# Kernel tuning notes

Measured on AMD Instinct MI355X. Metric: run time of the kernel, lower is better.

Reference implementation:

```python
import jax, jax.numpy as jnp
import numpy as np

N_NODES = 100000


def gcn_conv(x, src, dst, W, b, n_nodes):
    """PyG GCNConv: y = D^{-1/2} (A+I) D^{-1/2} (x W) + b, via edge scatter-add.
    src/dst already include self-loops."""
    xw = x @ W  # [N, out]
    ones = jnp.ones(dst.shape[0], dtype=xw.dtype)
    deg = jax.ops.segment_sum(ones, dst, num_segments=n_nodes)  # in-degree incl. self-loops
    dis = jnp.where(deg > 0, jax.lax.rsqrt(deg), 0.0)
    norm = dis[src] * dis[dst]  # [E]
    msgs = xw[src] * norm[:, None]  # [E, out] gather-scale
    out = jax.ops.segment_sum(msgs, dst, num_segments=n_nodes)
    return out + b


def setup_inputs() -> dict:
    key = jax.random.key(0)
    k1, k2, k3, k4, k5, k6 = jax.random.split(key, 6)
    n_features, hidden, n_classes = 128, 64, 16
    n_edges = 1600000
    x = jax.random.normal(k1, (N_NODES, n_features), dtype=jnp.float32)
    edge_index = jax.random.randint(k2, (2, n_edges), 0, N_NODES, dtype=jnp.int64)
    W1 = jax.random.normal(k3, (n_features, hidden), dtype=jnp.float32) / np.sqrt(n_features)
    b1 = jnp.zeros((hidden,), dtype=jnp.float32)
    W2 = jax.random.normal(k4, (hidden, n_classes), dtype=jnp.float32) / np.sqrt(hidden)
    b2 = jnp.zeros((n_classes,), dtype=jnp.float32)
    return {"x": x, "edge_index": edge_index, "W1": W1, "b1": b1, "W2": W2, "b2": b2}


def reference(x, edge_index, W1, b1, W2, b2):
    n = x.shape[0]
    # add self-loops once, shared by both layers (matches PyG default add_self_loops=True)
    loop = jnp.arange(n, dtype=edge_index.dtype)
    src = jnp.concatenate([edge_index[0], loop])
    dst = jnp.concatenate([edge_index[1], loop])
    h = gcn_conv(x, src, dst, W1, b1, n)
    h = jax.nn.relu(h)
    out = gcn_conv(h, src, dst, W2, b2, n)
    return out
```

## Files before the change

### kernel.cpp

```cpp
#include <hip/hip_runtime.h>
#include <hip/hip_fp16.h>

#define NF 128
#define NH 64
#define NC 16
#define NSLOT 48
#define G1ROWS 8
#define NPART 8

__global__ void k_init(int* __restrict__ cnt, int* __restrict__ binned, int n) {
    int i = blockIdx.x * blockDim.x + threadIdx.x;
    if (i < n) {
        cnt[i] = 1;
        binned[(size_t)i * NSLOT] = i;
    }
}

__global__ __launch_bounds__(256) void k_fill(const int* __restrict__ src,
                                              const int* __restrict__ dst,
                                              int* __restrict__ cnt,
                                              int* __restrict__ binned, int E, int psize) {
    int p  = blockIdx.x & (NPART - 1);
    int lo = p * psize, hi = lo + psize;
    int nb = gridDim.x >> 3, bi = blockIdx.x >> 3;
    int stride = nb * 256;
    for (int e = bi * 256 + threadIdx.x; e < E; e += stride) {
        int d = dst[e];
        if (d >= lo && d < hi) {
            int pos = atomicAdd(&cnt[d], 1);
            if (pos < NSLOT) binned[(size_t)d * NSLOT + pos] = src[e];
        }
    }
}

__global__ __launch_bounds__(256) void k_dis(const int* __restrict__ cnt,
                                             float* __restrict__ dis, int n) {
    int i = blockIdx.x * blockDim.x + threadIdx.x;
    if (i < n) dis[i] = 1.0f / sqrtf((float)cnt[i]);
}

__global__ __launch_bounds__(64, 4) void k_gemm1(const float* __restrict__ x,
                                                 const float* __restrict__ W1,
                                                 __half* __restrict__ xw, int n) {
    int c = threadIdx.x;
    int row0 = blockIdx.x * G1ROWS;
    const float* xp = x + (size_t)row0 * NF;
    float acc[G1ROWS] = {};
    if (row0 + G1ROWS <= n) {
        for (int k4 = 0; k4 < NF; k4 += 4) {
            float4 xv[G1ROWS];
#pragma unroll
            for (int r = 0; r < G1ROWS; ++r)
                xv[r] = *reinterpret_cast<const float4*>(xp + r * NF + k4);
#pragma unroll
            for (int kk = 0; kk < 4; ++kk) {
                float w = W1[(k4 + kk) * NH + c];
#pragma unroll
                for (int r = 0; r < G1ROWS; ++r) {
                    float xs = (kk == 0) ? xv[r].x : (kk == 1) ? xv[r].y
                             : (kk == 2) ? xv[r].z : xv[r].w;
                    acc[r] += xs * w;
                }
            }
        }
#pragma unroll
        for (int r = 0; r < G1ROWS; ++r)
            xw[(size_t)(row0 + r) * NH + c] = __float2half(acc[r]);
    } else {
        for (int k = 0; k < NF; ++k) {
            float w = W1[k * NH + c];
            for (int r = 0; r < G1ROWS; ++r)
                if (row0 + r < n) acc[r] += xp[r * NF + k] * w;
        }
        for (int r = 0; r < G1ROWS; ++r)
            if (row0 + r < n) xw[(size_t)(row0 + r) * NH + c] = __float2half(acc[r]);
    }
}

__global__ __launch_bounds__(256) void k_agg1(const int* __restrict__ cnt,
                                              const int* __restrict__ binned,
                                              const float* __restrict__ dis,
                                              const __half* __restrict__ xw,
                                              const float* __restrict__ b1,
                                              float* __restrict__ out1, int n) {
    int lane = threadIdx.x & 63;
    int g = lane >> 3;
    int w = lane & 7;
    int node = blockIdx.x * 4 + (threadIdx.x >> 6);
    if (node >= n) return;
    size_t off = (size_t)node * NSLOT;
    int dg = min(cnt[node], NSLOT);
    float acc[8] = {};
    for (int base = 0; base < dg; base += 8) {
        int j = base + g;
        if (j < dg) {
            int s = binned[off + j];
            float ds = dis[s];
            float4 raw = *reinterpret_cast<const float4*>(xw + (size_t)s * NH + w * 8);
            const __half2* h2 = reinterpret_cast<const __half2*>(&raw);
#pragma unroll
            for (int q = 0; q < 4; ++q) {
                float2 f = __half22float2(h2[q]);
                acc[2 * q]     += f.x * ds;
                acc[2 * q + 1] += f.y * ds;
            }
        }
    }
#pragma unroll
    for (int k = 0; k < 8; ++k) {
        acc[k] += __shfl_xor(acc[k], 8);
        acc[k] += __shfl_xor(acc[k], 16);
        acc[k] += __shfl_xor(acc[k], 32);
    }
    if (lane < 8) {
        float dn = dis[node];
        const float* bp = b1 + w * 8;
        float o[8];
#pragma unroll
        for (int k = 0; k < 8; ++k) o[k] = fmaxf(acc[k] * dn + bp[k], 0.f);
        float4* d4 = reinterpret_cast<float4*>(out1 + (size_t)node * NH + w * 8);
        d4[0] = make_float4(o[0], o[1], o[2], o[3]);
        d4[1] = make_float4(o[4], o[5], o[6], o[7]);
    }
}

__global__ __launch_bounds__(256, 8) void k_gemm2(const float* __restrict__ h_in,
                                                  const float* __restrict__ W2,
                                                  __half* __restrict__ hw, int n) {
    int lane = threadIdx.x & 63;
    int rsub = lane >> 4, c = lane & 15;
    int row0 = blockIdx.x * 64 + (threadIdx.x >> 6) * 16;
    float acc[4] = {0.f, 0.f, 0.f, 0.f};
    if (row0 + 16 <= n) {
#pragma unroll 2
        for (int k4 = 0; k4 < NH; k4 += 4) {
            float w0 = W2[(k4 + 0) * NC + c];
            float w1 = W2[(k4 + 1) * NC + c];
            float w2 = W2[(k4 + 2) * NC + c];
            float w3 = W2[(k4 + 3) * NC + c];
#pragma unroll
            for (int t = 0; t < 4; ++t) {
                float4 hv = *reinterpret_cast<const float4*>(
                    h_in + (size_t)(row0 + rsub + 4 * t) * NH + k4);
                acc[t] += hv.x * w0 + hv.y * w1 + hv.z * w2 + hv.w * w3;
            }
        }
#pragma unroll
        for (int t = 0; t < 4; ++t)
            hw[(size_t)(row0 + rsub + 4 * t) * NC + c] = __float2half(acc[t]);
    } else if (row0 < n) {
        for (int k = 0; k < NH; ++k) {
            float w = W2[k * NC + c];
            for (int t = 0; t < 4; ++t) {
                int row = row0 + rsub + 4 * t;
                if (row < n) acc[t] += h_in[(size_t)row * NH + k] * w;
            }
        }
        for (int t = 0; t < 4; ++t) {
            int row = row0 + rsub + 4 * t;
            if (row < n) hw[(size_t)row * NC + c] = __float2half(acc[t]);
        }
    }
}

__global__ __launch_bounds__(256) void k_agg2(const int* __restrict__ cnt,
                                              const int* __restrict__ binned,
                                              const float* __restrict__ dis,
                                              const __half* __restrict__ hw,
                                              const float* __restrict__ b2,
                                              float* __restrict__ out, int n) {
    int lane = threadIdx.x & 63;
    int g = lane >> 3;
    int w = lane & 7;
    int node = blockIdx.x * 4 + (threadIdx.x >> 6);
    if (node >= n) return;
    size_t off = (size_t)node * NSLOT;
    int dg = min(cnt[node], NSLOT);
    float a0 = 0.f, a1 = 0.f;
    for (int base = 0; base < dg; base += 8) {
        int j = base + g;
        if (j < dg) {
            int s = binned[off + j];
            float ds = dis[s];
            __half2 hv = *reinterpret_cast<const __half2*>(hw + (size_t)s * NC + w * 2);
            float2 f = __half22float2(hv);
            a0 += f.x * ds; a1 += f.y * ds;
        }
    }
    a0 += __shfl_xor(a0, 8);  a1 += __shfl_xor(a1, 8);
    a0 += __shfl_xor(a0, 16); a1 += __shfl_xor(a1, 16);
    a0 += __shfl_xor(a0, 32); a1 += __shfl_xor(a1, 32);
    if (lane < 8) {
        float dn = dis[node];
        float2 o = make_float2(a0 * dn + b2[2 * w], a1 * dn + b2[2 * w + 1]);
        *reinterpret_cast<float2*>(out + (size_t)node * NC + 2 * w) = o;
    }
}

extern "C" void kernel_launch(void* const* d_in, const int* in_sizes, int n_in,
                              void* d_out, int out_size, void* d_ws, size_t ws_size,
                              hipStream_t stream) {
    const float* x  = (const float*)d_in[0];
    const int*   ei = (const int*)d_in[1];
    const float* W1 = (const float*)d_in[2];
    const float* b1 = (const float*)d_in[3];
    const float* W2 = (const float*)d_in[4];
    const float* b2 = (const float*)d_in[5];
    float* out = (float*)d_out;

    int n = in_sizes[0] / NF;
    int E = in_sizes[1] / 2;
    const int* src = ei;
    const int* dst = ei + E;
    int psize = (n + NPART - 1) / NPART;

    char* ws = (char*)d_ws;
    size_t off = 0;
    auto alloc = [&](size_t bytes) {
        void* p = ws + off;
        off = (off + bytes + 255) & ~(size_t)255;
        return p;
    };
    int*    cnt    = (int*)alloc((size_t)n * 4);
    float*  dis    = (float*)alloc((size_t)n * 4);
    int*    binned = (int*)alloc((size_t)n * NSLOT * 4);
    __half* xw     = (__half*)alloc((size_t)n * NH * 2);
    float*  out1   = (float*)alloc((size_t)n * NH * 4);
    __half* hw     = xw;

    k_init <<<(n + 255) / 256, 256, 0, stream>>>(cnt, binned, n);
    k_fill <<<4096, 256, 0, stream>>>(src, dst, cnt, binned, E, psize);
    k_dis  <<<(n + 255) / 256, 256, 0, stream>>>(cnt, dis, n);
    k_gemm1<<<(n + G1ROWS - 1) / G1ROWS, 64, 0, stream>>>(x, W1, xw, n);
    k_agg1 <<<(n + 3) / 4, 256, 0, stream>>>(cnt, binned, dis, xw, b1, out1, n);
    k_gemm2<<<(n + 63) / 64, 256, 0, stream>>>(out1, W2, hw, n);
    k_agg2 <<<(n + 3) / 4, 256, 0, stream>>>(cnt, binned, dis, hw, b2, out, n);
}
```

Before: 332.1 us.

## Fuse layer-2 GEMM into layer-1 aggregation and drop init/dis kernels

The second linear layer (ReLU(h)·W2) now runs inside the first aggregation kernel, which has become a grid-stride loop that keeps W2 and b1 in registers. That removes the float32 hidden-activation buffer round trip and one launch. Self-loops are now added explicitly in both aggregations, so the init kernel becomes a memset. The degree-normalisation computation is folded into gemm1. In exchange the aggregation kernel uses more registers and extra shuffle reductions, and its grid is fixed at 2048 blocks.

```diff
diff --git a/kernel.cpp b/kernel.cpp
--- a/kernel.cpp
+++ b/kernel.cpp
@@ -7,14 +7,6 @@
 #define NSLOT 48
 #define G1ROWS 8
 #define NPART 8
-
-__global__ void k_init(int* __restrict__ cnt, int* __restrict__ binned, int n) {
-    int i = blockIdx.x * blockDim.x + threadIdx.x;
-    if (i < n) {
-        cnt[i] = 1;
-        binned[(size_t)i * NSLOT] = i;
-    }
-}
 
 __global__ __launch_bounds__(256) void k_fill(const int* __restrict__ src,
                                               const int* __restrict__ dst,
@@ -33,17 +25,15 @@
     }
 }
 
-__global__ __launch_bounds__(256) void k_dis(const int* __restrict__ cnt,
-                                             float* __restrict__ dis, int n) {
-    int i = blockIdx.x * blockDim.x + threadIdx.x;
-    if (i < n) dis[i] = 1.0f / sqrtf((float)cnt[i]);
-}
-
 __global__ __launch_bounds__(64, 4) void k_gemm1(const float* __restrict__ x,
                                                  const float* __restrict__ W1,
-                                                 __half* __restrict__ xw, int n) {
+                                                 __half* __restrict__ xw,
+                                                 const int* __restrict__ cnt,
+                                                 float* __restrict__ dis, int n) {
     int c = threadIdx.x;
     int row0 = blockIdx.x * G1ROWS;
+    if (c < G1ROWS && row0 + c < n)
+        dis[row0 + c] = 1.0f / sqrtf((float)(cnt[row0 + c] + 1));
     const float* xp = x + (size_t)row0 * NF;
     float acc[G1ROWS] = {};
     if (row0 + G1ROWS <= n) {
@@ -82,84 +72,65 @@
                                               const float* __restrict__ dis,
                                               const __half* __restrict__ xw,
                                               const float* __restrict__ b1,
-                                              float* __restrict__ out1, int n) {
+                                              const float* __restrict__ W2,
+                                              __half* __restrict__ hw, int n) {
     int lane = threadIdx.x & 63;
     int g = lane >> 3;
     int w = lane & 7;
-    int node = blockIdx.x * 4 + (threadIdx.x >> 6);
-    if (node >= n) return;
-    size_t off = (size_t)node * NSLOT;
-    int dg = min(cnt[node], NSLOT);
-    float acc[8] = {};
-    for (int base = 0; base < dg; base += 8) {
-        int j = base + g;
-        if (j < dg) {
-            int s = binned[off + j];
-            float ds = dis[s];
-            float4 raw = *reinterpret_cast<const float4*>(xw + (size_t)s * NH + w * 8);
+    float bp[8], w2a[8], w2b[8];
+#pragma unroll
+    for (int k = 0; k < 8; ++k) {
+        bp[k]  = b1[8 * w + k];
+        w2a[k] = W2[(8 * w + k) * NC + 2 * g];
+        w2b[k] = W2[(8 * w + k) * NC + 2 * g + 1];
+    }
+    int wid = threadIdx.x >> 6;
+    for (int node = blockIdx.x * 4 + wid; node < n; node += gridDim.x * 4) {
+        size_t off = (size_t)node * NSLOT;
+        int dg = min(cnt[node], NSLOT);
+        float dn = dis[node];
+        float acc[8] = {};
+        if (g == 0) {
+            float4 raw = *reinterpret_cast<const float4*>(xw + (size_t)node * NH + w * 8);
             const __half2* h2 = reinterpret_cast<const __half2*>(&raw);
 #pragma unroll
             for (int q = 0; q < 4; ++q) {
                 float2 f = __half22float2(h2[q]);
-                acc[2 * q]     += f.x * ds;
-                acc[2 * q + 1] += f.y * ds;
+                acc[2 * q] += f.x * dn; acc[2 * q + 1] += f.y * dn;
             }
         }
-    }
-#pragma unroll
-    for (int k = 0; k < 8; ++k) {
-        acc[k] += __shfl_xor(acc[k], 8);
-        acc[k] += __shfl_xor(acc[k], 16);
-        acc[k] += __shfl_xor(acc[k], 32);
-    }
-    if (lane < 8) {
-        float dn = dis[node];
-        const float* bp = b1 + w * 8;
-        float o[8];
-#pragma unroll
-        for (int k = 0; k < 8; ++k) o[k] = fmaxf(acc[k] * dn + bp[k], 0.f);
-        float4* d4 = reinterpret_cast<float4*>(out1 + (size_t)node * NH + w * 8);
-        d4[0] = make_float4(o[0], o[1], o[2], o[3]);
-        d4[1] = make_float4(o[4], o[5], o[6], o[7]);
-    }
-}
-
-__global__ __launch_bounds__(256, 8) void k_gemm2(const float* __restrict__ h_in,
-                                                  const float* __restrict__ W2,
-                                                  __half* __restrict__ hw, int n) {
-    int lane = threadIdx.x & 63;
-    int rsub = lane >> 4, c = lane & 15;
-    int row0 = blockIdx.x * 64 + (threadIdx.x >> 6) * 16;
-    float acc[4] = {0.f, 0.f, 0.f, 0.f};
-    if (row0 + 16 <= n) {
-#pragma unroll 2
-        for (int k4 = 0; k4 < NH; k4 += 4) {
-            float w0 = W2[(k4 + 0) * NC + c];
-            float w1 = W2[(k4 + 1) * NC + c];
-            float w2 = W2[(k4 + 2) * NC + c];
-            float w3 = W2[(k4 + 3) * NC + c];
-#pragma unroll
-            for (int t = 0; t < 4; ++t) {
-                float4 hv = *reinterpret_cast<const float4*>(
-                    h_in + (size_t)(row0 + rsub + 4 * t) * NH + k4);
-                acc[t] += hv.x * w0 + hv.y * w1 + hv.z * w2 + hv.w * w3;
+        for (int base = 0; base < dg; base += 8) {
+            int j = base + g;
+            if (j < dg) {
+                int s = binned[off + j];
+                float ds = dis[s];
+                float4 raw = *reinterpret_cast<const float4*>(xw + (size_t)s * NH + w * 8);
+                const __half2* h2 = reinterpret_cast<const __half2*>(&raw);
+#pragma unroll
+                for (int q = 0; q < 4; ++q) {
+                    float2 f = __half22float2(h2[q]);
+                    acc[2 * q] += f.x * ds; acc[2 * q + 1] += f.y * ds;
+                }
             }
         }
 #pragma unroll
-        for (int t = 0; t < 4; ++t)
-            hw[(size_t)(row0 + rsub + 4 * t) * NC + c] = __float2half(acc[t]);
-    } else if (row0 < n) {
-        for (int k = 0; k < NH; ++k) {
-            float w = W2[k * NC + c];
-            for (int t = 0; t < 4; ++t) {
-                int row = row0 + rsub + 4 * t;
-                if (row < n) acc[t] += h_in[(size_t)row * NH + k] * w;
-            }
-        }
-        for (int t = 0; t < 4; ++t) {
-            int row = row0 + rsub + 4 * t;
-            if (row < n) hw[(size_t)row * NC + c] = __float2half(acc[t]);
-        }
+        for (int k = 0; k < 8; ++k) {
+            acc[k] += __shfl_xor(acc[k], 8);
+            acc[k] += __shfl_xor(acc[k], 16);
+            acc[k] += __shfl_xor(acc[k], 32);
+        }
+        float p0 = 0.f, p1 = 0.f;
+#pragma unroll
+        for (int k = 0; k < 8; ++k) {
+            float h = fmaxf(acc[k] * dn + bp[k], 0.f);
+            p0 += h * w2a[k]; p1 += h * w2b[k];
+        }
+        p0 += __shfl_xor(p0, 1); p1 += __shfl_xor(p1, 1);
+        p0 += __shfl_xor(p0, 2); p1 += __shfl_xor(p1, 2);
+        p0 += __shfl_xor(p0, 4); p1 += __shfl_xor(p1, 4);
+        if (w == 0)
+            *reinterpret_cast<__half2*>(hw + (size_t)node * NC + 2 * g) =
+                __floats2half2_rn(p0, p1);
     }
 }
 
@@ -176,7 +147,13 @@
     if (node >= n) return;
     size_t off = (size_t)node * NSLOT;
     int dg = min(cnt[node], NSLOT);
+    float dn = dis[node];
     float a0 = 0.f, a1 = 0.f;
+    if (g == 0) {
+        __half2 hv = *reinterpret_cast<const __half2*>(hw + (size_t)node * NC + w * 2);
+        float2 f = __half22float2(hv);
+        a0 += f.x * dn; a1 += f.y * dn;
+    }
     for (int base = 0; base < dg; base += 8) {
         int j = base + g;
         if (j < dg) {
@@ -191,7 +168,6 @@
     a0 += __shfl_xor(a0, 16); a1 += __shfl_xor(a1, 16);
     a0 += __shfl_xor(a0, 32); a1 += __shfl_xor(a1, 32);
     if (lane < 8) {
-        float dn = dis[node];
         float2 o = make_float2(a0 * dn + b2[2 * w], a1 * dn + b2[2 * w + 1]);
         *reinterpret_cast<float2*>(out + (size_t)node * NC + 2 * w) = o;
     }
@@ -225,14 +201,11 @@
     float*  dis    = (float*)alloc((size_t)n * 4);
     int*    binned = (int*)alloc((size_t)n * NSLOT * 4);
     __half* xw     = (__half*)alloc((size_t)n * NH * 2);
-    float*  out1   = (float*)alloc((size_t)n * NH * 4);
-    __half* hw     = xw;
-
-    k_init <<<(n + 255) / 256, 256, 0, stream>>>(cnt, binned, n);
+    __half* hw     = (__half*)alloc((size_t)n * NC * 2);
+
+    hipMemsetAsync(cnt, 0, (size_t)n * 4, stream);
     k_fill <<<4096, 256, 0, stream>>>(src, dst, cnt, binned, E, psize);
-    k_dis  <<<(n + 255) / 256, 256, 0, stream>>>(cnt, dis, n);
-    k_gemm1<<<(n + G1ROWS - 1) / G1ROWS, 64, 0, stream>>>(x, W1, xw, n);
-    k_agg1 <<<(n + 3) / 4, 256, 0, stream>>>(cnt, binned, dis, xw, b1, out1, n);
-    k_gemm2<<<(n + 63) / 64, 256, 0, stream>>>(out1, W2, hw, n);
+    k_gemm1<<<(n + G1ROWS - 1) / G1ROWS, 64, 0, stream>>>(x, W1, xw, cnt, dis, n);
+    k_agg1 <<<2048, 256, 0, stream>>>(cnt, binned, dis, xw, b1, W2, hw, n);
     k_agg2 <<<(n + 3) / 4, 256, 0, stream>>>(cnt, binned, dis, hw, b2, out, n);
 }
```

Result: no change. 330.8 us (-0.4%).
